# Kernel optimization log

Hardware: AMD Instinct MI355X
Metric: run time of the kernel (lower is better)

## Reference

```python
import jax, jax.numpy as jnp
import numpy as np

VOCAB, EMBED, HIDDEN = 32000, 512, 1024
B, T = 8, 256

def setup_inputs() -> dict:
    key = jax.random.key(0)
    ks = jax.random.split(key, 5)
    x = jax.random.randint(ks[0], (B, T), 0, VOCAB)
    embedding = jax.random.normal(ks[1], (VOCAB, EMBED), dtype=jnp.float32)
    W_xh = jax.random.normal(ks[2], (EMBED, HIDDEN), dtype=jnp.float32) * 0.01
    W_hh = jax.random.normal(ks[3], (HIDDEN, HIDDEN), dtype=jnp.float32) * 0.01
    b_h = jnp.zeros((HIDDEN,), dtype=jnp.float32)
    W_hy = jax.random.normal(ks[4], (HIDDEN, VOCAB), dtype=jnp.float32) * 0.01
    b_y = jnp.zeros((VOCAB,), dtype=jnp.float32)
    return {"x": x, "embedding": embedding, "W_xh": W_xh, "W_hh": W_hh,
            "b_h": b_h, "W_hy": W_hy, "b_y": b_y}

def reference(x, embedding, W_xh, W_hh, b_h, W_hy, b_y):
    # x: [B,T] int ids
    emb = embedding[x]                      # [B,T,E]
    # Precompute input contribution for all steps: [B,T,H]
    xh = jnp.einsum('bte,eh->bth', emb, W_xh) + b_h
    h0 = jnp.zeros((x.shape[0], W_hh.shape[0]), dtype=emb.dtype)

    def step(h, xh_t):
        h = jnp.tanh(xh_t + h @ W_hh)       # [B,H]
        return h, h

    _, hs = jax.lax.scan(step, h0, jnp.swapaxes(xh, 0, 1))  # hs: [T,B,H]
    hs = jnp.swapaxes(hs, 0, 1)             # [B,T,H]
    # Output projection batched over all timesteps (same math as per-step)
    y = jnp.einsum('bth,hv->btv', hs, W_hy) + b_y  # [B,T,V]
    return y
```

## Files before the change

### kernel.cpp

```cpp
#include <hip/hip_runtime.h>
#include <hip/hip_bf16.h>

#define VOCAB 32000
#define EMBED 512
#define HIDDEN 1024
#define NB 8
#define NT 256
#define XH_ROWS 16

#define NCH 8
#define NMEM 32
#define RCOLS 32
#define NBLK_REC 256
#define NBLK_TR 128
#define TILES_PER_TR 250

typedef __attribute__((ext_vector_type(8))) short bf16x8;
typedef __attribute__((ext_vector_type(4))) float f32x4;
typedef __attribute__((ext_vector_type(4))) unsigned u32x4;

#define AS1 __attribute__((address_space(1)))
#define AS3 __attribute__((address_space(3)))

__device__ __forceinline__ unsigned short bf16_bits(float f) {
    __hip_bfloat16 b = __float2bfloat16(f);
    unsigned short s;
    __builtin_memcpy(&s, &b, 2);
    return s;
}
__device__ __forceinline__ float lo16f(unsigned u) { return __uint_as_float(u << 16); }
__device__ __forceinline__ float hi16f(unsigned u) { return __uint_as_float(u & 0xffff0000u); }

__global__ __launch_bounds__(256) void k_xh(const int* __restrict__ ids,
                                            const float* __restrict__ emb,
                                            const float* __restrict__ Wxh,
                                            const float* __restrict__ bh,
                                            float* __restrict__ xh) {
    __shared__ alignas(16) float embS[XH_ROWS][EMBED];
    __shared__ int idsS[XH_ROWS];
    const int tid = threadIdx.x;
    const int blk = blockIdx.x;
    if (tid < XH_ROWS) idsS[tid] = ids[blk * XH_ROWS + tid];
    __syncthreads();
    const float4* emb4 = (const float4*)emb;
#pragma unroll
    for (int rep = 0; rep < (XH_ROWS * EMBED / 4) / 256; ++rep) {
        const int lin = rep * 256 + tid;
        const int r = lin >> 7;
        const int e4 = lin & 127;
        *(float4*)&embS[r][e4 * 4] = emb4[(size_t)idsS[r] * (EMBED / 4) + e4];
    }
    __syncthreads();
    float4 acc[XH_ROWS] = {};
    const float4* W4 = (const float4*)Wxh;
    for (int e = 0; e < EMBED; ++e) {
        const float4 w = W4[(size_t)e * (HIDDEN / 4) + tid];
#pragma unroll
        for (int r = 0; r < XH_ROWS; ++r) {
            const float ev = embS[r][e];
            acc[r].x += ev * w.x; acc[r].y += ev * w.y;
            acc[r].z += ev * w.z; acc[r].w += ev * w.w;
        }
    }
    const float4 bv = ((const float4*)bh)[tid];
#pragma unroll
    for (int r = 0; r < XH_ROWS; ++r) {
        float4 o;
        o.x = acc[r].x + bv.x; o.y = acc[r].y + bv.y;
        o.z = acc[r].z + bv.z; o.w = acc[r].w + bv.w;
        ((float4*)xh)[(size_t)(blk * XH_ROWS + r) * (HIDDEN / 4) + tid] = o;
    }
}

__global__ __launch_bounds__(256, 1) void k_fused(const float* __restrict__ Whh,
                                                  const float* __restrict__ xh,
                                                  unsigned long long* __restrict__ hx,
                                                  __hip_bfloat16* __restrict__ hs,
                                                  const float* __restrict__ Why,
                                                  __hip_bfloat16* __restrict__ Wt) {
    __shared__ alignas(16) float smemF[9808];
    float* xhS = smemF;
    float* hS  = smemF + 8192;
    float* red = smemF + 9280;
    const int tid = threadIdx.x;
    const int bid = blockIdx.x;

    if (bid >= NBLK_REC) {
        const int tb = bid - NBLK_REC;
        const int cc = tid & 31;
        const int r0 = tid >> 5;
        const int tbase = tb * TILES_PER_TR;
        for (int rnd = 0; rnd < (TILES_PER_TR + 7) / 8; ++rnd) {
            const int base = rnd * 8;
            __syncthreads();
#pragma unroll
            for (int u = 0; u < 8; ++u) {
                const int i = base + u;
                if (i < TILES_PER_TR) {
                    const int g = tbase + i;
                    const int n0 = (g % 1000) * 32;
                    const int k0 = (g / 1000) * 32;
                    float* tile = smemF + u * 1056;
#pragma unroll
                    for (int rr = 0; rr < 4; ++rr) {
                        const int r = r0 + rr * 8;
                        tile[cc * 33 + r] = Why[(size_t)(k0 + r) * VOCAB + n0 + cc];
                    }
                }
            }
            __syncthreads();
#pragma unroll
            for (int u = 0; u < 8; ++u) {
                const int i = base + u;
                if (i < TILES_PER_TR) {
                    const int g = tbase + i;
                    const int n0 = (g % 1000) * 32;
                    const int k0 = (g / 1000) * 32;
                    float* tile = smemF + u * 1056;
#pragma unroll
                    for (int rr = 0; rr < 4; ++rr) {
                        const int n = r0 + rr * 8;
                        Wt[(size_t)(n0 + n) * HIDDEN + k0 + cc] = __float2bfloat16(tile[n * 33 + cc]);
                    }
                }
            }
        }
        return;
    }

    const int c = bid & (NCH - 1);
    const int m = bid >> 3;
    const int j0 = m * RCOLS;
    unsigned long long* hxc = hx + (size_t)c * 1024;

    if (tid < 16)
        __hip_atomic_store(&hxc[512 + m * 16 + tid], 0ull, __ATOMIC_RELAXED,
                           __HIP_MEMORY_SCOPE_AGENT);

    const int col2 = tid & 15;
    const int part = tid >> 4;

    u32x4 wreg[16];
#pragma unroll
    for (int j = 0; j < 16; ++j) {
        u32x4 q;
#pragma unroll
        for (int e = 0; e < 4; ++e) {
            const int i = part * 64 + 4 * j + e;
            const float2 wv = *(const float2*)&Whh[(size_t)i * HIDDEN + j0 + 2 * col2];
            q[e] = (unsigned)bf16_bits(wv.x) | ((unsigned)bf16_bits(wv.y) << 16);
        }
        wreg[j] = q;
    }
    for (int idx = tid; idx < NT * RCOLS; idx += 256) {
        const int t = idx >> 5;
        const int col = idx & 31;
        xhS[idx] = xh[(size_t)(c * NT + t) * HIDDEN + j0 + col];
    }
    __syncthreads();

    const f32x4* hv4 = (const f32x4*)&hS[part * 68];
    const int w0 = tid;
    const int w1 = tid + 256;
    const int pe0 = 2 * tid + 4 * (tid >> 5);

    for (int t = 0; t < NT; ++t) {
        unsigned long long* rbuf = hxc + ((t + 1) & 1) * 512;
        unsigned long long* wbuf = hxc + (t & 1) * 512;
        const unsigned long long tok = (unsigned long long)(unsigned)t;
        unsigned long long a = __hip_atomic_load(&rbuf[w0], __ATOMIC_RELAXED, __HIP_MEMORY_SCOPE_AGENT);
        unsigned long long b = __hip_atomic_load(&rbuf[w1], __ATOMIC_RELAXED, __HIP_MEMORY_SCOPE_AGENT);
        while (((a & 0xffffull) != tok) | ((b & 0xffffull) != tok)) {
            __builtin_amdgcn_s_sleep(1);
            if ((a & 0xffffull) != tok)
                a = __hip_atomic_load(&rbuf[w0], __ATOMIC_RELAXED, __HIP_MEMORY_SCOPE_AGENT);
            if ((b & 0xffffull) != tok)
                b = __hip_atomic_load(&rbuf[w1], __ATOMIC_RELAXED, __HIP_MEMORY_SCOPE_AGENT);
        }
        *(float2*)&hS[pe0] = make_float2(__uint_as_float(((unsigned)(a >> 16) & 0xffffu) << 16),
                                         __uint_as_float(((unsigned)(a >> 32) & 0xffffu) << 16));
        *(float2*)&hS[pe0 + 544] = make_float2(__uint_as_float(((unsigned)(b >> 16) & 0xffffu) << 16),
                                               __uint_as_float(((unsigned)(b >> 32) & 0xffffu) << 16));
        __syncthreads();
        float a0 = 0.f, a1 = 0.f;
#pragma unroll
        for (int j = 0; j < 16; ++j) {
            const u32x4 w4 = wreg[j];
            const f32x4 h4 = hv4[j];
            a0 = fmaf(lo16f(w4.x), h4.x, a0); a1 = fmaf(hi16f(w4.x), h4.x, a1);
            a0 = fmaf(lo16f(w4.y), h4.y, a0); a1 = fmaf(hi16f(w4.y), h4.y, a1);
            a0 = fmaf(lo16f(w4.z), h4.z, a0); a1 = fmaf(hi16f(w4.z), h4.z, a1);
            a0 = fmaf(lo16f(w4.w), h4.w, a0); a1 = fmaf(hi16f(w4.w), h4.w, a1);
        }
        red[part * 33 + 2 * col2]     = a0;
        red[part * 33 + 2 * col2 + 1] = a1;
        __syncthreads();
        if (tid < RCOLS) {
            float s = 0.f;
#pragma unroll
            for (int p = 0; p < 16; ++p) s += red[p * 33 + tid];
            const float v = tanhf(xhS[t * RCOLS + tid] + s);
            const unsigned hb = (unsigned)bf16_bits(v);
            ((unsigned short*)hs)[(size_t)(c * NT + t) * HIDDEN + j0 + tid] = (unsigned short)hb;
            const unsigned pb = (unsigned)__shfl_xor((int)hb, 1, 64);
            if ((tid & 1) == 0) {
                const unsigned long long wv = (unsigned long long)(unsigned)(t + 1)
                                            | ((unsigned long long)hb << 16)
                                            | ((unsigned long long)pb << 32);
                __hip_atomic_store(&wbuf[m * 16 + (tid >> 1)], wv, __ATOMIC_RELAXED,
                                   __HIP_MEMORY_SCOPE_AGENT);
            }
        }
    }
}

__global__ __launch_bounds__(512, 2) void k_proj(const unsigned short* __restrict__ A,
                                                 const unsigned short* __restrict__ Bt,
                                                 const float* __restrict__ by,
                                                 float* __restrict__ C) {
    __shared__ unsigned short LDS[4][16384];
    const int tid = threadIdx.x;
    const int wid = tid >> 6;
    const int lane = tid & 63;
    const int lin = blockIdx.x;
    const int swz = (lin & 7) * 125 + (lin >> 3);
    const int mt = swz & 7, nt = swz >> 3;
    const int m0 = mt * 256, n0 = nt * 256;
    const int wr = wid >> 2, wc = wid & 3;
    const int fr = lane & 15, fq = lane >> 4;
    const int srow = tid >> 3;
    const int sslot = tid & 7;

    f32x4 acc[8][4] = {};

#define STAGE(kt, bf)                                                                     \
    {                                                                                     \
        const unsigned short* Ag = A + (size_t)m0 * HIDDEN + (size_t)(kt) * 64;           \
        const unsigned short* Bg = Bt + (size_t)n0 * HIDDEN + (size_t)(kt) * 64;          \
        _Pragma("unroll")                                                                 \
        for (int j = 0; j < 4; ++j) {                                                     \
            const int r = j * 64 + srow;                                                  \
            const int ls = ((sslot ^ (r & 7)) * 8);                                       \
            __builtin_amdgcn_global_load_lds(                                             \
                (const AS1 unsigned*)(Ag + (size_t)r * HIDDEN + ls),                      \
                (AS3 unsigned*)(&LDS[(bf) * 2 + 0][j * 4096 + wid * 512]), 16, 0, 0);     \
        }                                                                                 \
        _Pragma("unroll")                                                                 \
        for (int j = 0; j < 4; ++j) {                                                     \
            const int r = j * 64 + srow;                                                  \
            const int ls = ((sslot ^ (r & 7)) * 8);                                       \
            __builtin_amdgcn_global_load_lds(                                             \
                (const AS1 unsigned*)(Bg + (size_t)r * HIDDEN + ls),                      \
                (AS3 unsigned*)(&LDS[(bf) * 2 + 1][j * 4096 + wid * 512]), 16, 0, 0);     \
        }                                                                                 \
    }

    STAGE(0, 0);
    STAGE(1, 1);

    int cur = 0;
    for (int kt = 0; kt < 16; ++kt) {
        if (kt < 15) { asm volatile("s_waitcnt vmcnt(8)" ::: "memory"); }
        else         { asm volatile("s_waitcnt vmcnt(0)" ::: "memory"); }
        __builtin_amdgcn_s_barrier();

        const unsigned short* Ab = &LDS[cur * 2 + 0][0];
        const unsigned short* Bb = &LDS[cur * 2 + 1][0];
        bf16x8 af[8][2], bg[4][2];
#pragma unroll
        for (int mi = 0; mi < 8; ++mi) {
            const int ra = wr * 128 + mi * 16 + fr;
            af[mi][0] = *(const bf16x8*)&Ab[ra * 64 + (((0 * 4 + fq) ^ (fr & 7)) * 8)];
        }
#pragma unroll
        for (int ni = 0; ni < 4; ++ni) {
            const int rb = wc * 64 + ni * 16 + fr;
            bg[ni][0] = *(const bf16x8*)&Bb[rb * 64 + (((0 * 4 + fq) ^ (fr & 7)) * 8)];
        }
#pragma unroll
        for (int mi = 0; mi < 8; ++mi) {
            const int ra = wr * 128 + mi * 16 + fr;
            af[mi][1] = *(const bf16x8*)&Ab[ra * 64 + (((1 * 4 + fq) ^ (fr & 7)) * 8)];
        }
#pragma unroll
        for (int ni = 0; ni < 4; ++ni) {
            const int rb = wc * 64 + ni * 16 + fr;
            bg[ni][1] = *(const bf16x8*)&Bb[rb * 64 + (((1 * 4 + fq) ^ (fr & 7)) * 8)];
        }
        asm volatile("s_waitcnt lgkmcnt(12)" ::: "memory");
        __builtin_amdgcn_sched_barrier(0);
        __builtin_amdgcn_s_setprio(1);
#pragma unroll
        for (int mi = 0; mi < 8; ++mi)
#pragma unroll
            for (int ni = 0; ni < 4; ++ni)
                acc[mi][ni] = __builtin_amdgcn_mfma_f32_16x16x32_bf16(af[mi][0], bg[ni][0], acc[mi][ni], 0, 0, 0);
        __builtin_amdgcn_s_setprio(0);
        asm volatile("s_waitcnt lgkmcnt(0)" ::: "memory");
        __builtin_amdgcn_sched_barrier(0);
        __builtin_amdgcn_s_barrier();

        if (kt < 14) STAGE(kt + 2, cur);

        __builtin_amdgcn_s_setprio(1);
#pragma unroll
        for (int mi = 0; mi < 8; ++mi)
#pragma unroll
            for (int ni = 0; ni < 4; ++ni)
                acc[mi][ni] = __builtin_amdgcn_mfma_f32_16x16x32_bf16(af[mi][1], bg[ni][1], acc[mi][ni], 0, 0, 0);
        __builtin_amdgcn_s_setprio(0);
        cur ^= 1;
    }
#undef STAGE

#pragma unroll
    for (int ni = 0; ni < 4; ++ni) {
        const int col = n0 + wc * 64 + ni * 16 + fr;
        const float bias = by[col];
#pragma unroll
        for (int mi = 0; mi < 8; ++mi) {
            const int row = m0 + wr * 128 + mi * 16 + fq * 4;
            float* cp = C + (size_t)row * VOCAB + col;
            cp[0]                 = acc[mi][ni][0] + bias;
            cp[(size_t)VOCAB]     = acc[mi][ni][1] + bias;
            cp[(size_t)2 * VOCAB] = acc[mi][ni][2] + bias;
            cp[(size_t)3 * VOCAB] = acc[mi][ni][3] + bias;
        }
    }
}

extern "C" void kernel_launch(void* const* d_in, const int* in_sizes, int n_in,
                              void* d_out, int out_size, void* d_ws, size_t ws_size,
                              hipStream_t stream) {
    const int*   x   = (const int*)d_in[0];
    const float* emb = (const float*)d_in[1];
    const float* Wxh = (const float*)d_in[2];
    const float* Whh = (const float*)d_in[3];
    const float* bh  = (const float*)d_in[4];
    const float* Why = (const float*)d_in[5];
    const float* by  = (const float*)d_in[6];
    float* y = (float*)d_out;

    char* ws = (char*)d_ws;
    const size_t off_xh = 0;
    const size_t off_hx = off_xh + (size_t)NB * NT * HIDDEN * 4;
    const size_t off_hs = off_hx + (size_t)NCH * 2 * 512 * 8;
    const size_t off_wt = off_hs + (size_t)NB * NT * HIDDEN * 2;
    const size_t need   = off_wt + (size_t)VOCAB * HIDDEN * 2;
    if (ws_size < need) return;

    float* xh = (float*)(ws + off_xh);
    unsigned long long* hx = (unsigned long long*)(ws + off_hx);
    __hip_bfloat16* hs = (__hip_bfloat16*)(ws + off_hs);
    __hip_bfloat16* Wt = (__hip_bfloat16*)(ws + off_wt);

    k_xh<<<dim3((NB * NT) / XH_ROWS), 256, 0, stream>>>(x, emb, Wxh, bh, xh);
    k_fused<<<dim3(NBLK_REC + NBLK_TR), 256, 0, stream>>>(Whh, xh, hx, hs, Why, Wt);
    k_proj<<<dim3((2048 / 256) * (VOCAB / 256)), 512, 0, stream>>>((const unsigned short*)hs,
                                                                   (const unsigned short*)Wt, by, y);
}
```

Before: 793.4 us.

## Fuse output projection into recurrence kernel, overlapping GEMM with the scan via epoch flags

Removes the separate projection kernel and adds 250 projection blocks to the fused persistent kernel. These blocks wait on per-chain, per-64-step epoch flags and on transpose-done flags, then run smaller MFMA GEMM tiles (64x128) as hidden states become available, overlapping the output projection with the sequential recurrence. hs and Wt stores become agent-scope atomic stores so they are visible across blocks, and a memset clears the flags each call. The trade-off: the projection loses the large double-buffered 256x256 tiles, and the kernel needs 634 blocks to be co-resident to avoid deadlock.

```diff
diff --git a/kernel.cpp b/kernel.cpp
--- a/kernel.cpp
+++ b/kernel.cpp
@@ -13,6 +13,7 @@
 #define RCOLS 32
 #define NBLK_REC 256
 #define NBLK_TR 128
+#define NBLK_PROJ 250
 #define TILES_PER_TR 250
 
 typedef __attribute__((ext_vector_type(8))) short bf16x8;
@@ -75,9 +76,13 @@
 __global__ __launch_bounds__(256, 1) void k_fused(const float* __restrict__ Whh,
                                                   const float* __restrict__ xh,
                                                   unsigned long long* __restrict__ hx,
-                                                  __hip_bfloat16* __restrict__ hs,
+                                                  unsigned* __restrict__ epoch,
+                                                  unsigned* __restrict__ trf,
+                                                  unsigned* __restrict__ hs32,
                                                   const float* __restrict__ Why,
-                                                  __hip_bfloat16* __restrict__ Wt) {
+                                                  __hip_bfloat16* __restrict__ Wt,
+                                                  const float* __restrict__ by,
+                                                  float* __restrict__ C) {
     __shared__ alignas(16) float smemF[9808];
     float* xhS = smemF;
     float* hS  = smemF + 8192;
@@ -85,7 +90,7 @@
     const int tid = threadIdx.x;
     const int bid = blockIdx.x;
 
-    if (bid >= NBLK_REC) {
+    if (bid >= NBLK_REC && bid < NBLK_REC + NBLK_TR) {
         const int tb = bid - NBLK_REC;
         const int cc = tid & 31;
         const int r0 = tid >> 5;
@@ -117,10 +122,109 @@
                     const int n0 = (g % 1000) * 32;
                     const int k0 = (g / 1000) * 32;
                     float* tile = smemF + u * 1056;
-#pragma unroll
-                    for (int rr = 0; rr < 4; ++rr) {
-                        const int n = r0 + rr * 8;
-                        Wt[(size_t)(n0 + n) * HIDDEN + k0 + cc] = __float2bfloat16(tile[n * 33 + cc]);
+                    unsigned* Wt32 = (unsigned*)Wt;
+#pragma unroll
+                    for (int rep = 0; rep < 2; ++rep) {
+                        const int s = rep * 256 + tid;
+                        const int n = s >> 4, cp = s & 15;
+                        const unsigned lo = (unsigned)bf16_bits(tile[n * 33 + 2 * cp]);
+                        const unsigned hi = (unsigned)bf16_bits(tile[n * 33 + 2 * cp + 1]);
+                        __hip_atomic_store(&Wt32[(((size_t)(n0 + n) * HIDDEN + k0) >> 1) + cp],
+                                           lo | (hi << 16), __ATOMIC_RELAXED,
+                                           __HIP_MEMORY_SCOPE_AGENT);
+                    }
+                }
+            }
+        }
+        asm volatile("s_waitcnt vmcnt(0)" ::: "memory");
+        __syncthreads();
+        if (tid == 0)
+            __hip_atomic_store(&trf[tb], 1u, __ATOMIC_RELAXED, __HIP_MEMORY_SCOPE_AGENT);
+        return;
+    }
+
+    if (bid >= NBLK_REC + NBLK_TR) {
+        const int nn = bid - (NBLK_REC + NBLK_TR);
+        unsigned short* Alds = (unsigned short*)smemF;
+        unsigned short* Blds = Alds + 4096;
+        const unsigned short* hsu = (const unsigned short*)hs32;
+        const unsigned short* Wtu = (const unsigned short*)Wt;
+        const int w = tid >> 6;
+        const int lane = tid & 63;
+        const int fr = lane & 15, fq = lane >> 4;
+        if (tid < NBLK_TR) {
+            while (__hip_atomic_load(&trf[tid], __ATOMIC_RELAXED, __HIP_MEMORY_SCOPE_AGENT) == 0u)
+                __builtin_amdgcn_s_sleep(16);
+        }
+        __syncthreads();
+        for (int q = 0; q < 4; ++q) {
+            for (int ci = 0; ci < 8; ++ci) {
+                const int c = (nn + ci) & 7;
+                if (tid < NMEM) {
+                    while (__hip_atomic_load(&epoch[(c * 4 + q) * 32 + tid], __ATOMIC_RELAXED,
+                                             __HIP_MEMORY_SCOPE_AGENT) == 0u)
+                        __builtin_amdgcn_s_sleep(16);
+                }
+                __syncthreads();
+                f32x4 acc[4][2] = {};
+                for (int kt = 0; kt < 16; ++kt) {
+                    const unsigned short* Ag = hsu + (size_t)(c * NT + q * 64) * HIDDEN + kt * 64;
+                    const unsigned short* Bg = Wtu + (size_t)(nn * 128) * HIDDEN + kt * 64;
+#pragma unroll
+                    for (int s2 = 0; s2 < 2; ++s2) {
+                        const int ch = s2 * 256 + tid;
+                        const int row = ch >> 3, ss = (ch & 7) ^ (row & 7);
+                        __builtin_amdgcn_global_load_lds(
+                            (const AS1 unsigned*)(Ag + (size_t)row * HIDDEN + ss * 8),
+                            (AS3 unsigned*)(Alds + (s2 * 256 + w * 64) * 8), 16, 0, 0);
+                    }
+#pragma unroll
+                    for (int s2 = 0; s2 < 4; ++s2) {
+                        const int ch = s2 * 256 + tid;
+                        const int row = ch >> 3, ss = (ch & 7) ^ (row & 7);
+                        __builtin_amdgcn_global_load_lds(
+                            (const AS1 unsigned*)(Bg + (size_t)row * HIDDEN + ss * 8),
+                            (AS3 unsigned*)(Blds + (s2 * 256 + w * 64) * 8), 16, 0, 0);
+                    }
+                    asm volatile("s_waitcnt vmcnt(0)" ::: "memory");
+                    __syncthreads();
+                    bf16x8 af[4][2], bf[2][2];
+#pragma unroll
+                    for (int mi = 0; mi < 4; ++mi) {
+                        const int ra = mi * 16 + fr;
+#pragma unroll
+                        for (int ks = 0; ks < 2; ++ks)
+                            af[mi][ks] = *(const bf16x8*)&Alds[ra * 64 + (((ks * 4 + fq) ^ (fr & 7)) * 8)];
+                    }
+#pragma unroll
+                    for (int ni = 0; ni < 2; ++ni) {
+                        const int rb = w * 32 + ni * 16 + fr;
+#pragma unroll
+                        for (int ks = 0; ks < 2; ++ks)
+                            bf[ni][ks] = *(const bf16x8*)&Blds[rb * 64 + (((ks * 4 + fq) ^ (fr & 7)) * 8)];
+                    }
+#pragma unroll
+                    for (int mi = 0; mi < 4; ++mi)
+#pragma unroll
+                        for (int ni = 0; ni < 2; ++ni) {
+                            acc[mi][ni] = __builtin_amdgcn_mfma_f32_16x16x32_bf16(af[mi][0], bf[ni][0], acc[mi][ni], 0, 0, 0);
+                            acc[mi][ni] = __builtin_amdgcn_mfma_f32_16x16x32_bf16(af[mi][1], bf[ni][1], acc[mi][ni], 0, 0, 0);
+                        }
+                    __syncthreads();
+                }
+                const int m0 = c * NT + q * 64;
+#pragma unroll
+                for (int ni = 0; ni < 2; ++ni) {
+                    const int col = nn * 128 + w * 32 + ni * 16 + fr;
+                    const float bias = by[col];
+#pragma unroll
+                    for (int mi = 0; mi < 4; ++mi) {
+                        const int row = m0 + mi * 16 + fq * 4;
+                        float* cp = C + (size_t)row * VOCAB + col;
+                        cp[0]                 = acc[mi][ni][0] + bias;
+                        cp[(size_t)VOCAB]     = acc[mi][ni][1] + bias;
+                        cp[(size_t)2 * VOCAB] = acc[mi][ni][2] + bias;
+                        cp[(size_t)3 * VOCAB] = acc[mi][ni][3] + bias;
                     }
                 }
             }
@@ -132,10 +236,6 @@
     const int m = bid >> 3;
     const int j0 = m * RCOLS;
     unsigned long long* hxc = hx + (size_t)c * 1024;
-
-    if (tid < 16)
-        __hip_atomic_store(&hxc[512 + m * 16 + tid], 0ull, __ATOMIC_RELAXED,
-                           __HIP_MEMORY_SCOPE_AGENT);
 
     const int col2 = tid & 15;
     const int part = tid >> 4;
@@ -177,6 +277,9 @@
             if ((b & 0xffffull) != tok)
                 b = __hip_atomic_load(&rbuf[w1], __ATOMIC_RELAXED, __HIP_MEMORY_SCOPE_AGENT);
         }
+        if (tid == 0 && t != 0 && (t & 63) == 0)
+            __hip_atomic_store(&epoch[(c * 4 + (t >> 6) - 1) * 32 + m], 1u,
+                               __ATOMIC_RELAXED, __HIP_MEMORY_SCOPE_AGENT);
         *(float2*)&hS[pe0] = make_float2(__uint_as_float(((unsigned)(a >> 16) & 0xffffu) << 16),
                                          __uint_as_float(((unsigned)(a >> 32) & 0xffffu) << 16));
         *(float2*)&hS[pe0 + 544] = make_float2(__uint_as_float(((unsigned)(b >> 16) & 0xffffu) << 16),
@@ -201,9 +304,10 @@
             for (int p = 0; p < 16; ++p) s += red[p * 33 + tid];
             const float v = tanhf(xhS[t * RCOLS + tid] + s);
             const unsigned hb = (unsigned)bf16_bits(v);
-            ((unsigned short*)hs)[(size_t)(c * NT + t) * HIDDEN + j0 + tid] = (unsigned short)hb;
             const unsigned pb = (unsigned)__shfl_xor((int)hb, 1, 64);
             if ((tid & 1) == 0) {
+                __hip_atomic_store(&hs32[((size_t)(c * NT + t) * HIDDEN + j0 + tid) >> 1],
+                                   hb | (pb << 16), __ATOMIC_RELAXED, __HIP_MEMORY_SCOPE_AGENT);
                 const unsigned long long wv = (unsigned long long)(unsigned)(t + 1)
                                             | ((unsigned long long)hb << 16)
                                             | ((unsigned long long)pb << 32);
@@ -211,122 +315,13 @@
                                    __HIP_MEMORY_SCOPE_AGENT);
             }
         }
-    }
-}
-
-__global__ __launch_bounds__(512, 2) void k_proj(const unsigned short* __restrict__ A,
-                                                 const unsigned short* __restrict__ Bt,
-                                                 const float* __restrict__ by,
-                                                 float* __restrict__ C) {
-    __shared__ unsigned short LDS[4][16384];
-    const int tid = threadIdx.x;
-    const int wid = tid >> 6;
-    const int lane = tid & 63;
-    const int lin = blockIdx.x;
-    const int swz = (lin & 7) * 125 + (lin >> 3);
-    const int mt = swz & 7, nt = swz >> 3;
-    const int m0 = mt * 256, n0 = nt * 256;
-    const int wr = wid >> 2, wc = wid & 3;
-    const int fr = lane & 15, fq = lane >> 4;
-    const int srow = tid >> 3;
-    const int sslot = tid & 7;
-
-    f32x4 acc[8][4] = {};
-
-#define STAGE(kt, bf)                                                                     \
-    {                                                                                     \
-        const unsigned short* Ag = A + (size_t)m0 * HIDDEN + (size_t)(kt) * 64;           \
-        const unsigned short* Bg = Bt + (size_t)n0 * HIDDEN + (size_t)(kt) * 64;          \
-        _Pragma("unroll")                                                                 \
-        for (int j = 0; j < 4; ++j) {                                                     \
-            const int r = j * 64 + srow;                                                  \
-            const int ls = ((sslot ^ (r & 7)) * 8);                                       \
-            __builtin_amdgcn_global_load_lds(                                             \
-                (const AS1 unsigned*)(Ag + (size_t)r * HIDDEN + ls),                      \
-                (AS3 unsigned*)(&LDS[(bf) * 2 + 0][j * 4096 + wid * 512]), 16, 0, 0);     \
-        }                                                                                 \
-        _Pragma("unroll")                                                                 \
-        for (int j = 0; j < 4; ++j) {                                                     \
-            const int r = j * 64 + srow;                                                  \
-            const int ls = ((sslot ^ (r & 7)) * 8);                                       \
-            __builtin_amdgcn_global_load_lds(                                             \
-                (const AS1 unsigned*)(Bg + (size_t)r * HIDDEN + ls),                      \
-                (AS3 unsigned*)(&LDS[(bf) * 2 + 1][j * 4096 + wid * 512]), 16, 0, 0);     \
-        }                                                                                 \
-    }
-
-    STAGE(0, 0);
-    STAGE(1, 1);
-
-    int cur = 0;
-    for (int kt = 0; kt < 16; ++kt) {
-        if (kt < 15) { asm volatile("s_waitcnt vmcnt(8)" ::: "memory"); }
-        else         { asm volatile("s_waitcnt vmcnt(0)" ::: "memory"); }
-        __builtin_amdgcn_s_barrier();
-
-        const unsigned short* Ab = &LDS[cur * 2 + 0][0];
-        const unsigned short* Bb = &LDS[cur * 2 + 1][0];
-        bf16x8 af[8][2], bg[4][2];
-#pragma unroll
-        for (int mi = 0; mi < 8; ++mi) {
-            const int ra = wr * 128 + mi * 16 + fr;
-            af[mi][0] = *(const bf16x8*)&Ab[ra * 64 + (((0 * 4 + fq) ^ (fr & 7)) * 8)];
-        }
-#pragma unroll
-        for (int ni = 0; ni < 4; ++ni) {
-            const int rb = wc * 64 + ni * 16 + fr;
-            bg[ni][0] = *(const bf16x8*)&Bb[rb * 64 + (((0 * 4 + fq) ^ (fr & 7)) * 8)];
-        }
-#pragma unroll
-        for (int mi = 0; mi < 8; ++mi) {
-            const int ra = wr * 128 + mi * 16 + fr;
-            af[mi][1] = *(const bf16x8*)&Ab[ra * 64 + (((1 * 4 + fq) ^ (fr & 7)) * 8)];
-        }
-#pragma unroll
-        for (int ni = 0; ni < 4; ++ni) {
-            const int rb = wc * 64 + ni * 16 + fr;
-            bg[ni][1] = *(const bf16x8*)&Bb[rb * 64 + (((1 * 4 + fq) ^ (fr & 7)) * 8)];
-        }
-        asm volatile("s_waitcnt lgkmcnt(12)" ::: "memory");
-        __builtin_amdgcn_sched_barrier(0);
-        __builtin_amdgcn_s_setprio(1);
-#pragma unroll
-        for (int mi = 0; mi < 8; ++mi)
-#pragma unroll
-            for (int ni = 0; ni < 4; ++ni)
-                acc[mi][ni] = __builtin_amdgcn_mfma_f32_16x16x32_bf16(af[mi][0], bg[ni][0], acc[mi][ni], 0, 0, 0);
-        __builtin_amdgcn_s_setprio(0);
-        asm volatile("s_waitcnt lgkmcnt(0)" ::: "memory");
-        __builtin_amdgcn_sched_barrier(0);
-        __builtin_amdgcn_s_barrier();
-
-        if (kt < 14) STAGE(kt + 2, cur);
-
-        __builtin_amdgcn_s_setprio(1);
-#pragma unroll
-        for (int mi = 0; mi < 8; ++mi)
-#pragma unroll
-            for (int ni = 0; ni < 4; ++ni)
-                acc[mi][ni] = __builtin_amdgcn_mfma_f32_16x16x32_bf16(af[mi][1], bg[ni][1], acc[mi][ni], 0, 0, 0);
-        __builtin_amdgcn_s_setprio(0);
-        cur ^= 1;
-    }
-#undef STAGE
-
-#pragma unroll
-    for (int ni = 0; ni < 4; ++ni) {
-        const int col = n0 + wc * 64 + ni * 16 + fr;
-        const float bias = by[col];
-#pragma unroll
-        for (int mi = 0; mi < 8; ++mi) {
-            const int row = m0 + wr * 128 + mi * 16 + fq * 4;
-            float* cp = C + (size_t)row * VOCAB + col;
-            cp[0]                 = acc[mi][ni][0] + bias;
-            cp[(size_t)VOCAB]     = acc[mi][ni][1] + bias;
-            cp[(size_t)2 * VOCAB] = acc[mi][ni][2] + bias;
-            cp[(size_t)3 * VOCAB] = acc[mi][ni][3] + bias;
-        }
-    }
+        asm volatile("" ::: "memory");
+    }
+    asm volatile("s_waitcnt vmcnt(0)" ::: "memory");
+    __syncthreads();
+    if (tid == 0)
+        __hip_atomic_store(&epoch[(c * 4 + 3) * 32 + m], 1u, __ATOMIC_RELAXED,
+                           __HIP_MEMORY_SCOPE_AGENT);
 }
 
 extern "C" void kernel_launch(void* const* d_in, const int* in_sizes, int n_in,
@@ -344,18 +339,22 @@
     char* ws = (char*)d_ws;
     const size_t off_xh = 0;
     const size_t off_hx = off_xh + (size_t)NB * NT * HIDDEN * 4;
-    const size_t off_hs = off_hx + (size_t)NCH * 2 * 512 * 8;
+    const size_t off_ep = off_hx + (size_t)NCH * 2 * 512 * 8;
+    const size_t off_tf = off_ep + 8 * 4 * 32 * 4;
+    const size_t off_hs = off_hx + 0x20000;
     const size_t off_wt = off_hs + (size_t)NB * NT * HIDDEN * 2;
     const size_t need   = off_wt + (size_t)VOCAB * HIDDEN * 2;
     if (ws_size < need) return;
 
     float* xh = (float*)(ws + off_xh);
     unsigned long long* hx = (unsigned long long*)(ws + off_hx);
-    __hip_bfloat16* hs = (__hip_bfloat16*)(ws + off_hs);
+    unsigned* epoch = (unsigned*)(ws + off_ep);
+    unsigned* trf = (unsigned*)(ws + off_tf);
+    unsigned* hs32 = (unsigned*)(ws + off_hs);
     __hip_bfloat16* Wt = (__hip_bfloat16*)(ws + off_wt);
 
+    hipMemsetAsync(ws + off_hx, 0, 0x20000, stream);
     k_xh<<<dim3((NB * NT) / XH_ROWS), 256, 0, stream>>>(x, emb, Wxh, bh, xh);
-    k_fused<<<dim3(NBLK_REC + NBLK_TR), 256, 0, stream>>>(Whh, xh, hx, hs, Why, Wt);
-    k_proj<<<dim3((2048 / 256) * (VOCAB / 256)), 512, 0, stream>>>((const unsigned short*)hs,
-                                                                   (const unsigned short*)Wt, by, y);
+    k_fused<<<dim3(NBLK_REC + NBLK_TR + NBLK_PROJ), 256, 0, stream>>>(
+        Whh, xh, hx, epoch, trf, hs32, Why, Wt, by, y);
 }
```

New measurement: 861.9 us. 8.6% more time.
